# Optimization experiments

Hardware: AMD Instinct MI355X
Metric: run time of the kernel (lower is better)

## Reference

```python
import jax, jax.numpy as jnp
import numpy as np


def setup_inputs() -> dict:
    key = jax.random.key(0)
    k1, k2, k3 = jax.random.split(key, 3)
    N, F, E, H = 50000, 256, 800000, 4
    P = F // H + 1            # proj = 65
    dk = P * H                # 260
    x = jax.random.normal(k1, (N, F), dtype=jnp.float32)
    W = jax.random.normal(k2, (2 * dk, F), dtype=jnp.float32) * 0.02
    b = jnp.zeros((2 * dk,), dtype=jnp.float32)
    edge_index = jax.random.randint(k3, (2, E), 0, N, dtype=jnp.int32)
    return {"x": x, "edge_index": edge_index, "W": W, "b": b, "num_heads": H}


def reference(x, edge_index, W, b, num_heads):
    # x: [N, F]; W: [2*dk, F] with dk = P*num_heads; edge_index: [2, E]
    N = x.shape[0]
    P = W.shape[0] // (2 * num_heads)
    qk = x @ W.T + b                                   # [N, 2*dk]
    qk = qk.reshape(N, num_heads, 2 * P)               # 'L (h hdim) -> L h hdim'
    q, k = qk[..., :P], qk[..., P:]                    # split=2 outer -> q then k, each [N, H, P]
    src, dst = edge_index[0], edge_index[1]
    # per-edge dot product per head (NB: original never applies self.scale)
    scores = jnp.einsum('ehp,ehp->eh', q[src], k[dst])  # [E, H]
    # sparse softmax over dim=2 (columns) i.e. segment-softmax grouped by row index per head
    smax = jax.ops.segment_max(scores, src, num_segments=N)  # [N, H]
    ex = jnp.exp(scores - smax[src])                         # [E, H]
    denom = jax.ops.segment_sum(ex, src, num_segments=N)     # [N, H]
    attn = ex / denom[src]                                   # [E, H]
    # torch.sparse.sum(attn, dim=0) / num_heads -> mean over heads per edge
    vals = attn.mean(axis=1)                                 # [E]
    return vals
```

## Files before the change

kernel.cpp:

```cpp
#include <hip/hip_runtime.h>
#include <hip/hip_bf16.h>

#define K_DIM 256
#define RQ    512
#define NPAD  640
#define GBM 128
#define GBN 128
#define GBK 32
#define EPITCH 152
#define NBK   104
#define CBLK  256
#define SBAND 12512
#define DBAND 25024

typedef unsigned short u16;
using short8  = __attribute__((ext_vector_type(8))) short;
using ushort8 = __attribute__((ext_vector_type(8))) unsigned short;
using f32x4   = __attribute__((ext_vector_type(4))) float;
using f32x2   = __attribute__((ext_vector_type(2))) float;

__device__ __forceinline__ float asf(unsigned u) {
  union { unsigned i; float f; } x; x.i = u; return x.f;
}
__device__ __forceinline__ u16 f2b(float f) {
  __hip_bfloat16 h = __float2bfloat16(f); return *(u16*)&h;
}
__device__ __forceinline__ u16 f2h(float f) { _Float16 h = (_Float16)f; return *(u16*)&h; }
__device__ __forceinline__ float h2f(u16 u) { _Float16 h = *(_Float16*)&u; return (float)h; }

__device__ __forceinline__ int bucket_of(int s, int d) {
  int sband = s / SBAND;
  int dband = d / DBAND;
  int ssub  = (s - sband * SBAND) >> 10;
  return ((sband << 1) | dband) * 13 + ssub;
}

__device__ __forceinline__ int map2(int p) {
  if (p < 256) return (p >> 6) * 130 + (p & 63);
  if (p < 512) { int q = p - 256; return (q >> 6) * 130 + 65 + (q & 63); }
  if (p < 516) return (p - 512) * 130 + 64;
  if (p < 520) return (p - 516) * 130 + 129;
  return -1;
}

__global__ void __launch_bounds__(256) prep(
    const float* __restrict__ x, const float* __restrict__ W,
    const float* __restrict__ bv, const int* __restrict__ ei,
    u16* __restrict__ xb, u16* __restrict__ wb,
    float* __restrict__ bias, float* __restrict__ zbase,
    int* __restrict__ counts,
    int M, int Mpad, int E, int per, int xblocks, int wblocks, int zblocks)
{
  __shared__ int h[NBK];
  const int blk = blockIdx.x, tid = threadIdx.x;
  if (blk < xblocks) {
    int idx = blk * 256 + tid;
    int total = Mpad * (K_DIM / 8);
    if (idx >= total) return;
    int row = idx / (K_DIM / 8);
    ushort8 o;
    if (row < M) {
      const float* s = x + (size_t)idx * 8;
      float4 a = *(const float4*)s;
      float4 b = *(const float4*)(s + 4);
      o[0] = f2b(a.x); o[1] = f2b(a.y); o[2] = f2b(a.z); o[3] = f2b(a.w);
      o[4] = f2b(b.x); o[5] = f2b(b.y); o[6] = f2b(b.z); o[7] = f2b(b.w);
    } else {
      #pragma unroll
      for (int j = 0; j < 8; ++j) o[j] = 0;
    }
    *(ushort8*)(xb + (size_t)idx * 8) = o;
  } else if (blk < xblocks + wblocks) {
    int idx = (blk - xblocks) * 256 + tid;
    int total = NPAD * (K_DIM / 8);
    if (idx >= total) return;
    int p  = idx / (K_DIM / 8);
    int kc = (idx % (K_DIM / 8)) * 8;
    int c  = map2(p);
    ushort8 o;
    if (c >= 0) {
      const float* s = W + (size_t)c * K_DIM + kc;
      float4 a = *(const float4*)s;
      float4 v = *(const float4*)(s + 4);
      o[0] = f2b(a.x); o[1] = f2b(a.y); o[2] = f2b(a.z); o[3] = f2b(a.w);
      o[4] = f2b(v.x); o[5] = f2b(v.y); o[6] = f2b(v.z); o[7] = f2b(v.w);
    } else {
      #pragma unroll
      for (int j = 0; j < 8; ++j) o[j] = 0;
    }
    *(ushort8*)(wb + (size_t)idx * 8) = o;
    if (kc == 0) bias[p] = (c >= 0) ? bv[c] : 0.f;
  } else if (blk < xblocks + wblocks + zblocks) {
    int i = (blk - xblocks - wblocks) * 256 + tid;
    if (i < M * 4) zbase[i] = 0.f;
  } else {
    int cb = blk - xblocks - wblocks - zblocks;
    if (tid < NBK) h[tid] = 0;
    __syncthreads();
    int start = cb * per, end = min(start + per, E);
    for (int i = start + tid; i < end; i += 256)
      atomicAdd(&h[bucket_of(ei[i], ei[E + i])], 1);
    __syncthreads();
    if (tid < NBK) counts[tid * CBLK + cb] = h[tid];
  }
}

__global__ void __launch_bounds__(256) gemm_mfma(
    const u16* __restrict__ xb, const u16* __restrict__ wb,
    const float* __restrict__ bias, u16* __restrict__ qkb,
    u16* __restrict__ tl, int M)
{
  __shared__ u16 smem[GBM * EPITCH];
  const int tid  = threadIdx.x;
  const int wave = tid >> 6, lane = tid & 63;
  const int l15 = lane & 15, lhi = lane >> 4;
  const int row0 = blockIdx.x * GBM, p0 = blockIdx.y * GBN;
  const int wr = (wave >> 1) * 64, wc = (wave & 1) * 64;

  f32x4 acc[4][4];
  #pragma unroll
  for (int m = 0; m < 4; ++m)
    #pragma unroll
    for (int n = 0; n < 4; ++n) acc[m][n] = (f32x4){0.f, 0.f, 0.f, 0.f};

#define STAGE(b, k0) do {                                                     \
    u16* As_ = smem + (b) * 8192;                                             \
    u16* Bs_ = As_ + 4096;                                                    \
    _Pragma("unroll")                                                         \
    for (int i_ = 0; i_ < 2; ++i_) {                                          \
      int f_ = wave * 128 + i_ * 64 + lane;                                   \
      int r_ = f_ >> 2, c_ = f_ & 3;                                          \
      const u16* gA = xb + (size_t)(row0 + r_) * K_DIM + (k0) + c_ * 8;       \
      __builtin_amdgcn_global_load_lds(                                       \
          (const __attribute__((address_space(1))) void*)gA,                  \
          (__attribute__((address_space(3))) void*)(As_ + (wave*128 + i_*64)*8), \
          16, 0, 0);                                                          \
      const u16* gB = wb + (size_t)(p0 + r_) * K_DIM + (k0) + c_ * 8;         \
      __builtin_amdgcn_global_load_lds(                                       \
          (const __attribute__((address_space(1))) void*)gB,                  \
          (__attribute__((address_space(3))) void*)(Bs_ + (wave*128 + i_*64)*8), \
          16, 0, 0);                                                          \
    }                                                                         \
  } while (0)

  STAGE(0, 0);
  asm volatile("s_waitcnt vmcnt(0)" ::: "memory");
  __syncthreads();

  #pragma unroll
  for (int t = 0; t < K_DIM / GBK; ++t) {
    if (t < K_DIM / GBK - 1) STAGE((t + 1) & 1, (t + 1) * GBK);
    const u16* As = smem + (t & 1) * 8192;
    const u16* Bs = As + 4096;
    short8 af[4], bf[4];
    #pragma unroll
    for (int m = 0; m < 4; ++m)
      af[m] = *(const short8*)(As + (size_t)(wr + m * 16 + l15) * GBK + lhi * 8);
    #pragma unroll
    for (int n = 0; n < 4; ++n)
      bf[n] = *(const short8*)(Bs + (size_t)(wc + n * 16 + l15) * GBK + lhi * 8);
    #pragma unroll
    for (int m = 0; m < 4; ++m)
      #pragma unroll
      for (int n = 0; n < 4; ++n)
        acc[m][n] = __builtin_amdgcn_mfma_f32_16x16x32_bf16(af[m], bf[n], acc[m][n], 0, 0, 0);
    if (t < K_DIM / GBK - 1) {
      asm volatile("s_waitcnt vmcnt(0)" ::: "memory");
      __syncthreads();
    }
  }
#undef STAGE

  __syncthreads();

  #pragma unroll
  for (int n = 0; n < 4; ++n) {
    int col = wc + n * 16 + l15;
    float bvv = bias[p0 + col];
    #pragma unroll
    for (int m = 0; m < 4; ++m) {
      #pragma unroll
      for (int r = 0; r < 4; ++r) {
        int row = wr + m * 16 + lhi * 4 + r;
        smem[row * EPITCH + col] = f2b(acc[m][n][r] + bvv);
      }
    }
  }
  __syncthreads();

  if (p0 < 512) {
    #pragma unroll
    for (int it = 0; it < 8; ++it) {
      int row  = wave * 32 + it * 4 + lhi;
      int grow = row0 + row;
      uint4 v = *(const uint4*)(smem + row * EPITCH + l15 * 8);
      if (grow < M)
        *(uint4*)(qkb + (size_t)grow * RQ + p0 + l15 * 8) = v;
    }
  } else {
    #pragma unroll
    for (int it = 0; it < 8; ++it) {
      int row  = wave * 32 + it * 4 + lhi;
      int grow = row0 + row;
      if (l15 == 0 && grow < M) {
        uint4 v = *(const uint4*)(smem + row * EPITCH);
        *(uint4*)(tl + (size_t)grow * 8) = v;
      }
    }
  }
}

__global__ void __launch_bounds__(1024) scan_k(int* __restrict__ counts)
{
  __shared__ int tot[NBK], base[NBK];
  const int tid = threadIdx.x, wv = tid >> 6, ln = tid & 63;
  for (int k = wv; k < NBK; k += 16) {
    int sum = 0;
    #pragma unroll
    for (int c = 0; c < CBLK / 64; ++c) sum += counts[k * CBLK + c * 64 + ln];
    #pragma unroll
    for (int off = 1; off < 64; off <<= 1) sum += __shfl_xor(sum, off);
    if (ln == 0) tot[k] = sum;
  }
  __syncthreads();
  if (tid == 0) {
    int run = 0;
    for (int k = 0; k < NBK; ++k) { base[k] = run; run += tot[k]; }
  }
  __syncthreads();
  for (int k = wv; k < NBK; k += 16) {
    int carry = base[k];
    #pragma unroll
    for (int c = 0; c < CBLK / 64; ++c) {
      int v = counts[k * CBLK + c * 64 + ln];
      int inc = v;
      #pragma unroll
      for (int off = 1; off < 64; off <<= 1) {
        int u = __shfl_up(inc, off);
        if (ln >= off) inc += u;
      }
      int last = __shfl(inc, 63);
      counts[k * CBLK + c * 64 + ln] = carry + inc - v;
      carry += last;
    }
  }
}

__global__ void __launch_bounds__(256) scatter2_k(
    const int* __restrict__ ei, const int* __restrict__ offs,
    uint2* __restrict__ sorted, int E, int per)
{
  __shared__ int cur[NBK];
  const int tid = threadIdx.x, blk = blockIdx.x;
  if (tid < NBK) cur[tid] = offs[tid * CBLK + blk];
  __syncthreads();
  int start = blk * per, end = min(start + per, E);
  for (int i = start + tid; i < end; i += 256) {
    int s = ei[i], d = ei[E + i];
    int pos = atomicAdd(&cur[bucket_of(s, d)], 1);
    sorted[pos] = make_uint2(((unsigned)s << 16) | (unsigned)d, (unsigned)i);
  }
}

__global__ void __launch_bounds__(256, 4) edge_pass(
    const u16* __restrict__ qkb, const u16* __restrict__ tl,
    const uint2* __restrict__ sorted,
    u16* __restrict__ exh, float* __restrict__ denom, int E)
{
  const int tid  = threadIdx.x;
  const int wave = tid >> 6, lane = tid & 63;
  const int g = lane >> 3;
  const int l = lane & 7;

  const int nwg = gridDim.x;
  const int q8 = nwg >> 3, r8 = nwg & 7;
  const int xcd = blockIdx.x & 7, bix = blockIdx.x >> 3;
  const int swz = (xcd < r8) ? (xcd * (q8 + 1) + bix)
                             : (r8 * (q8 + 1) + (xcd - r8) * q8 + bix);

  const int s0 = swz * 64 + wave * 16 + g;
  const int s1 = s0 + 8;
  const bool v0 = s0 < E, v1 = s1 < E;
  uint2 r0 = sorted[v0 ? s0 : 0];
  uint2 r1 = sorted[v1 ? s1 : 0];
  const int src0 = r0.x >> 16, dst0 = r0.x & 0xffff;
  const int src1 = r1.x >> 16, dst1 = r1.x & 0xffff;

  const u16* q0p = qkb + (size_t)src0 * RQ + l * 32;
  const u16* k0p = qkb + (size_t)dst0 * RQ + 256 + l * 32;
  const u16* q1p = qkb + (size_t)src1 * RQ + l * 32;
  const u16* k1p = qkb + (size_t)dst1 * RQ + 256 + l * 32;

  uint4 qv0[4], kv0[4], qv1[4], kv1[4];
  #pragma unroll
  for (int c = 0; c < 4; ++c) {
    qv0[c] = *(const uint4*)(q0p + c * 8);
    kv0[c] = *(const uint4*)(k0p + c * 8);
  }
  #pragma unroll
  for (int c = 0; c < 4; ++c) {
    qv1[c] = *(const uint4*)(q1p + c * 8);
    kv1[c] = *(const uint4*)(k1p + c * 8);
  }
  int2 t0 = make_int2(0, 0), t1 = make_int2(0, 0);
  if (l < 2) {
    t0 = *(const int2*)(tl + (size_t)(l ? dst0 : src0) * 8 + (l ? 4 : 0));
    t1 = *(const int2*)(tl + (size_t)(l ? dst1 : src1) * 8 + (l ? 4 : 0));
  }

  const int h = l >> 1;
  const int idxA = ((g << 3) | (l & 1)) << 2;

#define EDGE_COMPUTE(qv, kv, ti, src_, e_, vld) do {                          \
    f32x2 a2 = {0.f, 0.f};                                                    \
    _Pragma("unroll")                                                         \
    for (int c = 0; c < 4; ++c) {                                             \
      const unsigned* qd = (const unsigned*)&qv[c];                           \
      const unsigned* kd = (const unsigned*)&kv[c];                           \
      _Pragma("unroll")                                                       \
      for (int j = 0; j < 4; ++j) {                                           \
        f32x2 qa = { asf(qd[j] << 16), asf(qd[j] & 0xffff0000u) };            \
        f32x2 ka = { asf(kd[j] << 16), asf(kd[j] & 0xffff0000u) };            \
        a2 += qa * ka;                                                        \
      }                                                                       \
    }                                                                         \
    float s = a2[0] + a2[1];                                                  \
    s += __shfl_xor(s, 1);                                                    \
    int w01 = __builtin_amdgcn_ds_bpermute(idxA, ti.x);                       \
    int w23 = __builtin_amdgcn_ds_bpermute(idxA, ti.y);                       \
    unsigned wsel = (h & 2) ? (unsigned)w23 : (unsigned)w01;                  \
    float tv = (h & 1) ? asf(wsel & 0xffff0000u) : asf(wsel << 16);           \
    float to = __shfl_xor(tv, 1);                                             \
    s = fmaf(tv, to, s);                                                      \
    float ev = __expf(s);                                                     \
    if ((vld) && (l & 1) == 0) {                                              \
      exh[(size_t)(e_) * 4 + h] = f2h(ev);                                    \
      unsafeAtomicAdd(&denom[(size_t)(src_) * 4 + h], ev);                    \
    }                                                                         \
  } while (0)

  EDGE_COMPUTE(qv0, kv0, t0, src0, r0.y, v0);
  EDGE_COMPUTE(qv1, kv1, t1, src1, r1.y, v1);
#undef EDGE_COMPUTE
}

__global__ void __launch_bounds__(256) finalize_k(
    const u16* __restrict__ exh, const float* __restrict__ denom,
    const int* __restrict__ ei, float* __restrict__ out, int E)
{
  int e = blockIdx.x * 256 + threadIdx.x;
  if (e >= E) return;
  int src = ei[e];
  ushort4 ev = *(const ushort4*)(exh + (size_t)e * 4);
  float4 dv = *(const float4*)(denom + (size_t)src * 4);
  out[e] = 0.25f * (h2f(ev.x) / dv.x + h2f(ev.y) / dv.y
                  + h2f(ev.z) / dv.z + h2f(ev.w) / dv.w);
}

extern "C" void kernel_launch(void* const* d_in, const int* in_sizes, int n_in,
                              void* d_out, int out_size, void* d_ws, size_t ws_size,
                              hipStream_t stream)
{
  const float* x  = (const float*)d_in[0];
  const int*   ei = (const int*)d_in[1];
  const float* W  = (const float*)d_in[2];
  const float* b  = (const float*)d_in[3];

  const int F = in_sizes[2] / in_sizes[3];
  const int M = in_sizes[0] / F;
  const int E = in_sizes[1] / 2;

  const int mblocks = (M + GBM - 1) / GBM;
  const int Mpad    = mblocks * GBM;

  u16* xb  = (u16*)d_ws;
  u16* wb  = xb + (size_t)Mpad * K_DIM;
  u16* qkb = wb + (size_t)NPAD * K_DIM;
  u16* tl  = qkb + (size_t)M * RQ;
  float* bias  = (float*)(tl + (size_t)M * 8);
  u16*   exh   = (u16*)(bias + NPAD);
  float* denom = (float*)(exh + (size_t)E * 4);
  int*   counts = (int*)(denom + (size_t)M * 4);
  uint2* sorted = (uint2*)(counts + NBK * CBLK);

  const int xblocks = (Mpad * (K_DIM / 8) + 255) / 256;
  const int wblocks = (NPAD * (K_DIM / 8) + 255) / 256;
  const int zblocks = (M * 4 + 255) / 256;
  const int per     = (E + CBLK - 1) / CBLK;
  hipLaunchKernelGGL(prep, dim3(xblocks + wblocks + zblocks + CBLK), dim3(256), 0,
                     stream, x, W, b, ei, xb, wb, bias, denom, counts,
                     M, Mpad, E, per, xblocks, wblocks, zblocks);

  hipLaunchKernelGGL(scan_k, dim3(1), dim3(1024), 0, stream, counts);

  dim3 gg(mblocks, NPAD / GBN);
  hipLaunchKernelGGL(gemm_mfma, gg, dim3(256), 0, stream, xb, wb, bias, qkb, tl, M);

  hipLaunchKernelGGL(scatter2_k, dim3(CBLK), dim3(256), 0, stream,
                     ei, counts, sorted, E, per);

  int eblocks = (E + 63) / 64;
  hipLaunchKernelGGL(edge_pass, dim3(eblocks), dim3(256), 0, stream,
                     qkb, tl, sorted, exh, denom, E);

  hipLaunchKernelGGL(finalize_k, dim3((E + 255) / 256), dim3(256), 0, stream,
                     exh, denom, ei, (float*)d_out, E);
}
```

Baseline: 168.8 us.

## Fuse scatter into GEMM launch, memset denom, process three edges per group

The edge scatter kernel now runs as extra blocks of the GEMM launch using a 1D grid, which removes one kernel launch and lets scatter overlap with the GEMM tail. Zeroing of the denominator moves from prep blocks to hipMemsetAsync. The edge pass handles three edges per 8-lane group instead of two, with occupancy lowered to 3 waves/SIMD, to get more memory-level parallelism per thread at the cost of registers. The added memset is an extra operation in the stream.

```diff
diff --git a/kernel.cpp b/kernel.cpp
--- a/kernel.cpp
+++ b/kernel.cpp
@@ -47,9 +47,8 @@
     const float* __restrict__ x, const float* __restrict__ W,
     const float* __restrict__ bv, const int* __restrict__ ei,
     u16* __restrict__ xb, u16* __restrict__ wb,
-    float* __restrict__ bias, float* __restrict__ zbase,
-    int* __restrict__ counts,
-    int M, int Mpad, int E, int per, int xblocks, int wblocks, int zblocks)
+    float* __restrict__ bias, int* __restrict__ counts,
+    int M, int Mpad, int E, int per, int xblocks, int wblocks)
 {
   __shared__ int h[NBK];
   const int blk = blockIdx.x, tid = threadIdx.x;
@@ -90,11 +89,8 @@
     }
     *(ushort8*)(wb + (size_t)idx * 8) = o;
     if (kc == 0) bias[p] = (c >= 0) ? bv[c] : 0.f;
-  } else if (blk < xblocks + wblocks + zblocks) {
-    int i = (blk - xblocks - wblocks) * 256 + tid;
-    if (i < M * 4) zbase[i] = 0.f;
   } else {
-    int cb = blk - xblocks - wblocks - zblocks;
+    int cb = blk - xblocks - wblocks;
     if (tid < NBK) h[tid] = 0;
     __syncthreads();
     int start = cb * per, end = min(start + per, E);
@@ -105,16 +101,70 @@
   }
 }
 
-__global__ void __launch_bounds__(256) gemm_mfma(
+__global__ void __launch_bounds__(1024) scan_k(int* __restrict__ counts)
+{
+  __shared__ int tot[NBK], base[NBK];
+  const int tid = threadIdx.x, wv = tid >> 6, ln = tid & 63;
+  for (int k = wv; k < NBK; k += 16) {
+    int sum = 0;
+    #pragma unroll
+    for (int c = 0; c < CBLK / 64; ++c) sum += counts[k * CBLK + c * 64 + ln];
+    #pragma unroll
+    for (int off = 1; off < 64; off <<= 1) sum += __shfl_xor(sum, off);
+    if (ln == 0) tot[k] = sum;
+  }
+  __syncthreads();
+  if (tid == 0) {
+    int run = 0;
+    for (int k = 0; k < NBK; ++k) { base[k] = run; run += tot[k]; }
+  }
+  __syncthreads();
+  for (int k = wv; k < NBK; k += 16) {
+    int carry = base[k];
+    #pragma unroll
+    for (int c = 0; c < CBLK / 64; ++c) {
+      int v = counts[k * CBLK + c * 64 + ln];
+      int inc = v;
+      #pragma unroll
+      for (int off = 1; off < 64; off <<= 1) {
+        int u = __shfl_up(inc, off);
+        if (ln >= off) inc += u;
+      }
+      int last = __shfl(inc, 63);
+      counts[k * CBLK + c * 64 + ln] = carry + inc - v;
+      carry += last;
+    }
+  }
+}
+
+__global__ void __launch_bounds__(256) gemm_scatter(
     const u16* __restrict__ xb, const u16* __restrict__ wb,
     const float* __restrict__ bias, u16* __restrict__ qkb,
-    u16* __restrict__ tl, int M)
+    u16* __restrict__ tl, int M,
+    const int* __restrict__ ei, const int* __restrict__ offs,
+    uint2* __restrict__ sorted, int E, int per, int gemmBlocks, int mblocks)
 {
   __shared__ u16 smem[GBM * EPITCH];
-  const int tid  = threadIdx.x;
+  const int tid = threadIdx.x;
+
+  if (blockIdx.x >= gemmBlocks) {
+    int* cur = (int*)smem;
+    const int blk = blockIdx.x - gemmBlocks;
+    if (tid < NBK) cur[tid] = offs[tid * CBLK + blk];
+    __syncthreads();
+    int start = blk * per, end = min(start + per, E);
+    for (int i = start + tid; i < end; i += 256) {
+      int s = ei[i], d = ei[E + i];
+      int pos = atomicAdd(&cur[bucket_of(s, d)], 1);
+      sorted[pos] = make_uint2(((unsigned)s << 16) | (unsigned)d, (unsigned)i);
+    }
+    return;
+  }
+
   const int wave = tid >> 6, lane = tid & 63;
   const int l15 = lane & 15, lhi = lane >> 4;
-  const int row0 = blockIdx.x * GBM, p0 = blockIdx.y * GBN;
+  const int row0 = (blockIdx.x % mblocks) * GBM;
+  const int p0   = (blockIdx.x / mblocks) * GBN;
   const int wr = (wave >> 1) * 64, wc = (wave & 1) * 64;
 
   f32x4 acc[4][4];
@@ -210,59 +260,7 @@
   }
 }
 
-__global__ void __launch_bounds__(1024) scan_k(int* __restrict__ counts)
-{
-  __shared__ int tot[NBK], base[NBK];
-  const int tid = threadIdx.x, wv = tid >> 6, ln = tid & 63;
-  for (int k = wv; k < NBK; k += 16) {
-    int sum = 0;
-    #pragma unroll
-    for (int c = 0; c < CBLK / 64; ++c) sum += counts[k * CBLK + c * 64 + ln];
-    #pragma unroll
-    for (int off = 1; off < 64; off <<= 1) sum += __shfl_xor(sum, off);
-    if (ln == 0) tot[k] = sum;
-  }
-  __syncthreads();
-  if (tid == 0) {
-    int run = 0;
-    for (int k = 0; k < NBK; ++k) { base[k] = run; run += tot[k]; }
-  }
-  __syncthreads();
-  for (int k = wv; k < NBK; k += 16) {
-    int carry = base[k];
-    #pragma unroll
-    for (int c = 0; c < CBLK / 64; ++c) {
-      int v = counts[k * CBLK + c * 64 + ln];
-      int inc = v;
-      #pragma unroll
-      for (int off = 1; off < 64; off <<= 1) {
-        int u = __shfl_up(inc, off);
-        if (ln >= off) inc += u;
-      }
-      int last = __shfl(inc, 63);
-      counts[k * CBLK + c * 64 + ln] = carry + inc - v;
-      carry += last;
-    }
-  }
-}
-
-__global__ void __launch_bounds__(256) scatter2_k(
-    const int* __restrict__ ei, const int* __restrict__ offs,
-    uint2* __restrict__ sorted, int E, int per)
-{
-  __shared__ int cur[NBK];
-  const int tid = threadIdx.x, blk = blockIdx.x;
-  if (tid < NBK) cur[tid] = offs[tid * CBLK + blk];
-  __syncthreads();
-  int start = blk * per, end = min(start + per, E);
-  for (int i = start + tid; i < end; i += 256) {
-    int s = ei[i], d = ei[E + i];
-    int pos = atomicAdd(&cur[bucket_of(s, d)], 1);
-    sorted[pos] = make_uint2(((unsigned)s << 16) | (unsigned)d, (unsigned)i);
-  }
-}
-
-__global__ void __launch_bounds__(256, 4) edge_pass(
+__global__ void __launch_bounds__(256, 3) edge_pass(
     const u16* __restrict__ qkb, const u16* __restrict__ tl,
     const uint2* __restrict__ sorted,
     u16* __restrict__ exh, float* __restrict__ denom, int E)
@@ -278,34 +276,38 @@
   const int swz = (xcd < r8) ? (xcd * (q8 + 1) + bix)
                              : (r8 * (q8 + 1) + (xcd - r8) * q8 + bix);
 
-  const int s0 = swz * 64 + wave * 16 + g;
+  const int s0 = swz * 96 + wave * 24 + g;
   const int s1 = s0 + 8;
-  const bool v0 = s0 < E, v1 = s1 < E;
+  const int s2 = s0 + 16;
+  const bool v0 = s0 < E, v1 = s1 < E, v2 = s2 < E;
   uint2 r0 = sorted[v0 ? s0 : 0];
   uint2 r1 = sorted[v1 ? s1 : 0];
+  uint2 r2 = sorted[v2 ? s2 : 0];
   const int src0 = r0.x >> 16, dst0 = r0.x & 0xffff;
   const int src1 = r1.x >> 16, dst1 = r1.x & 0xffff;
-
-  const u16* q0p = qkb + (size_t)src0 * RQ + l * 32;
-  const u16* k0p = qkb + (size_t)dst0 * RQ + 256 + l * 32;
-  const u16* q1p = qkb + (size_t)src1 * RQ + l * 32;
-  const u16* k1p = qkb + (size_t)dst1 * RQ + 256 + l * 32;
-
-  uint4 qv0[4], kv0[4], qv1[4], kv1[4];
+  const int src2 = r2.x >> 16, dst2 = r2.x & 0xffff;
+
+  uint4 qv0[4], kv0[4], qv1[4], kv1[4], qv2[4], kv2[4];
   #pragma unroll
   for (int c = 0; c < 4; ++c) {
-    qv0[c] = *(const uint4*)(q0p + c * 8);
-    kv0[c] = *(const uint4*)(k0p + c * 8);
+    qv0[c] = *(const uint4*)(qkb + (size_t)src0 * RQ + l * 32 + c * 8);
+    kv0[c] = *(const uint4*)(qkb + (size_t)dst0 * RQ + 256 + l * 32 + c * 8);
   }
   #pragma unroll
   for (int c = 0; c < 4; ++c) {
-    qv1[c] = *(const uint4*)(q1p + c * 8);
-    kv1[c] = *(const uint4*)(k1p + c * 8);
-  }
-  int2 t0 = make_int2(0, 0), t1 = make_int2(0, 0);
+    qv1[c] = *(const uint4*)(qkb + (size_t)src1 * RQ + l * 32 + c * 8);
+    kv1[c] = *(const uint4*)(qkb + (size_t)dst1 * RQ + 256 + l * 32 + c * 8);
+  }
+  #pragma unroll
+  for (int c = 0; c < 4; ++c) {
+    qv2[c] = *(const uint4*)(qkb + (size_t)src2 * RQ + l * 32 + c * 8);
+    kv2[c] = *(const uint4*)(qkb + (size_t)dst2 * RQ + 256 + l * 32 + c * 8);
+  }
+  int2 t0 = make_int2(0, 0), t1 = make_int2(0, 0), t2 = make_int2(0, 0);
   if (l < 2) {
     t0 = *(const int2*)(tl + (size_t)(l ? dst0 : src0) * 8 + (l ? 4 : 0));
     t1 = *(const int2*)(tl + (size_t)(l ? dst1 : src1) * 8 + (l ? 4 : 0));
+    t2 = *(const int2*)(tl + (size_t)(l ? dst2 : src2) * 8 + (l ? 4 : 0));
   }
 
   const int h = l >> 1;
@@ -341,6 +343,7 @@
 
   EDGE_COMPUTE(qv0, kv0, t0, src0, r0.y, v0);
   EDGE_COMPUTE(qv1, kv1, t1, src1, r1.y, v1);
+  EDGE_COMPUTE(qv2, kv2, t2, src2, r2.y, v2);
 #undef EDGE_COMPUTE
 }
 
@@ -385,21 +388,22 @@
 
   const int xblocks = (Mpad * (K_DIM / 8) + 255) / 256;
   const int wblocks = (NPAD * (K_DIM / 8) + 255) / 256;
-  const int zblocks = (M * 4 + 255) / 256;
   const int per     = (E + CBLK - 1) / CBLK;
-  hipLaunchKernelGGL(prep, dim3(xblocks + wblocks + zblocks + CBLK), dim3(256), 0,
-                     stream, x, W, b, ei, xb, wb, bias, denom, counts,
-                     M, Mpad, E, per, xblocks, wblocks, zblocks);
+
+  hipMemsetAsync(denom, 0, (size_t)M * 4 * sizeof(float), stream);
+
+  hipLaunchKernelGGL(prep, dim3(xblocks + wblocks + CBLK), dim3(256), 0,
+                     stream, x, W, b, ei, xb, wb, bias, counts,
+                     M, Mpad, E, per, xblocks, wblocks);
 
   hipLaunchKernelGGL(scan_k, dim3(1), dim3(1024), 0, stream, counts);
 
-  dim3 gg(mblocks, NPAD / GBN);
-  hipLaunchKernelGGL(gemm_mfma, gg, dim3(256), 0, stream, xb, wb, bias, qkb, tl, M);
-
-  hipLaunchKernelGGL(scatter2_k, dim3(CBLK), dim3(256), 0, stream,
-                     ei, counts, sorted, E, per);
-
-  int eblocks = (E + 63) / 64;
+  const int gemmBlocks = mblocks * (NPAD / GBN);
+  hipLaunchKernelGGL(gemm_scatter, dim3(gemmBlocks + CBLK), dim3(256), 0, stream,
+                     xb, wb, bias, qkb, tl, M,
+                     ei, counts, sorted, E, per, gemmBlocks, mblocks);
+
+  int eblocks = (E + 95) / 96;
   hipLaunchKernelGGL(edge_pass, dim3(eblocks), dim3(256), 0, stream,
                      qkb, tl, sorted, exh, denom, E);
 
```

After: 170.8 us. No clear change (+1.2%).
